# Kernel optimization log

Hardware: AMD Instinct MI355X
Metric: run time of the kernel (lower is better)

## Reference

```python
import math
import jax, jax.numpy as jnp
import numpy as np

D_MODEL = 1024
NUM_HEADS = 16
HEAD_DIM = D_MODEL // NUM_HEADS
BATCH = 4
SEQ = 2048


def setup_inputs() -> dict:
    key = jax.random.key(0)
    ks = jax.random.split(key, 9)
    scale = 1.0 / math.sqrt(D_MODEL)
    return {
        "x": jax.random.normal(ks[0], (BATCH, SEQ, D_MODEL), dtype=jnp.float32),
        "wq": jax.random.normal(ks[1], (D_MODEL, D_MODEL), dtype=jnp.float32) * scale,
        "bq": jnp.zeros((D_MODEL,), dtype=jnp.float32),
        "wk": jax.random.normal(ks[2], (D_MODEL, D_MODEL), dtype=jnp.float32) * scale,
        "bk": jnp.zeros((D_MODEL,), dtype=jnp.float32),
        "wv": jax.random.normal(ks[3], (D_MODEL, D_MODEL), dtype=jnp.float32) * scale,
        "bv": jnp.zeros((D_MODEL,), dtype=jnp.float32),
        "wo": jax.random.normal(ks[4], (D_MODEL, D_MODEL), dtype=jnp.float32) * scale,
        "bo": jnp.zeros((D_MODEL,), dtype=jnp.float32),
    }


def _split_heads(t):
    b, s, _ = t.shape
    return t.reshape(b, s, NUM_HEADS, HEAD_DIM).transpose(0, 2, 1, 3)  # [b,h,s,d]


def reference(x, wq, bq, wk, bk, wv, bv, wo, bo):
    # Linear layers: y = x @ W^T + b (torch nn.Linear convention)
    q = _split_heads(x @ wq.T + bq)
    k = _split_heads(x @ wk.T + bk)
    v = _split_heads(x @ wv.T + bv)
    scores = jnp.einsum("bhqd,bhkd->bhqk", q, k) / math.sqrt(HEAD_DIM)
    attn_weights = jax.nn.softmax(scores, axis=-1)  # dropout=0.0 (eval) -> identity
    context = jnp.einsum("bhqk,bhkd->bhqd", attn_weights, v)
    context = context.transpose(0, 2, 1, 3).reshape(x.shape[0], x.shape[1], D_MODEL)
    output = context @ wo.T + bo
    return output, attn_weights
```

## Files before the change

### kernel.cpp

```cpp
#include <hip/hip_runtime.h>
#include <cstdint>
#include <cstddef>


#define D_MODEL 1024
#define NHEADS  16
#define HDIM    64
#define BATCH   4
#define SEQ     2048
#define NTOK    (BATCH*SEQ)

typedef __bf16 bf16x8 __attribute__((ext_vector_type(8)));
typedef float  f32x4  __attribute__((ext_vector_type(4)));
typedef unsigned short u16x8 __attribute__((ext_vector_type(8)));

__device__ __forceinline__ uint16_t f2bf(float f) {
  union { float f; uint32_t u; } v; v.f = f;
  return (uint16_t)((v.u + 0x7FFFu + ((v.u >> 16) & 1u)) >> 16);
}
__device__ __forceinline__ float bf2f(uint16_t u) {
  union { uint32_t u; float f; } v; v.u = (uint32_t)u << 16; return v.f;
}
__device__ __forceinline__ bf16x8 ldbf8(const uint16_t* p) {
  return __builtin_bit_cast(bf16x8, *(const u16x8*)p);
}
__device__ __forceinline__ void nt_store4(float* p, float a, float b, float c, float d) {
  f32x4 v = { a, b, c, d };
  __builtin_nontemporal_store(v, (f32x4*)p);
}
#define MFMA16(a, b, c) __builtin_amdgcn_mfma_f32_16x16x32_bf16((a), (b), (c), 0, 0, 0)

__device__ __forceinline__ void gl_lds16(const uint16_t* g, uint16_t* l) {
  __builtin_amdgcn_global_load_lds(
      (const __attribute__((address_space(1))) uint32_t*)g,
      (__attribute__((address_space(3))) uint32_t*)l, 16, 0, 0);
}

__global__ __launch_bounds__(256) void cvt_kernel(const float* __restrict__ src,
                                                  uint16_t* __restrict__ dst, int n4) {
  int i = blockIdx.x * blockDim.x + threadIdx.x;
  if (i < n4) {
    float4 f = ((const float4*)src)[i];
    ushort4 o;
    o.x = f2bf(f.x); o.y = f2bf(f.y); o.z = f2bf(f.z); o.w = f2bf(f.w);
    ((ushort4*)dst)[i] = o;
  }
}
__global__ __launch_bounds__(256)
void cvt_w_kernel(const float* __restrict__ wq, const float* __restrict__ wk,
                  const float* __restrict__ wv, const float* __restrict__ wo,
                  uint16_t* __restrict__ dst) {
  int i = blockIdx.x * blockDim.x + threadIdx.x;
  int sel = i >> 18, off = i & 262143;
  const float* src = (sel == 0) ? wq : (sel == 1) ? wk : (sel == 2) ? wv : wo;
  float4 f = ((const float4*)src)[off];
  ushort4 o;
  o.x = f2bf(f.x); o.y = f2bf(f.y); o.z = f2bf(f.z); o.w = f2bf(f.w);
  ((ushort4*)dst)[i] = o;
}

__global__ __launch_bounds__(256)
void gemm_qkv(const uint16_t* __restrict__ A, const uint16_t* __restrict__ Wqkv,
              const float* __restrict__ bq, const float* __restrict__ bk,
              const float* __restrict__ bv,
              uint16_t* __restrict__ Qb, uint16_t* __restrict__ Kc,
              uint16_t* __restrict__ Vt) {
  __shared__ uint16_t As[128 * 64];
  __shared__ uint16_t Bs[128 * 64];
  const int flat = blockIdx.x;
  const int l = (flat & 7) * 192 + (flat >> 3);
  const int bx = l % 24, by = l / 24;
  const int tid  = threadIdx.x;
  const int lane = tid & 63;
  const int wave = tid >> 6;
  const int wr = wave >> 1, wc = wave & 1;
  const int m0 = by * 128, n0 = bx * 128;
  const int lrow = lane & 15;
  const int grp  = lane >> 4;
  const int l8   = lane >> 3;
  const int c8   = lane & 7;

  f32x4 acc[4][4] = {};

  for (int k0 = 0; k0 < 1024; k0 += 64) {
#pragma unroll
    for (int it = 0; it < 4; ++it) {
      const int chunk = wave * 4 + it;
      const int row = chunk * 8 + l8;
      gl_lds16(&A   [(size_t)(m0 + row) * 1024 + k0 + c8 * 8], &As[chunk * 512]);
      gl_lds16(&Wqkv[(size_t)(n0 + row) * 1024 + k0 + c8 * 8], &Bs[chunk * 512]);
    }
    __syncthreads();
#pragma unroll
    for (int ks = 0; ks < 2; ++ks) {
      bf16x8 af[4], bfr[4];
#pragma unroll
      for (int i = 0; i < 4; ++i) {
        af [i] = ldbf8(&As[(wr * 64 + i * 16 + lrow) * 64 + ks * 32 + grp * 8]);
        bfr[i] = ldbf8(&Bs[(wc * 64 + i * 16 + lrow) * 64 + ks * 32 + grp * 8]);
      }
#pragma unroll
      for (int i = 0; i < 4; ++i)
#pragma unroll
        for (int j = 0; j < 4; ++j)
          acc[i][j] = MFMA16(af[i], bfr[j], acc[i][j]);
    }
    __syncthreads();
  }

  const int seg = n0 >> 10;
  const float* bp = (seg == 0) ? bq : (seg == 1) ? bk : bv;
  uint16_t* dst01 = (seg == 0) ? Qb : Kc;
  const int r0 = grp * 4;
#pragma unroll
  for (int i = 0; i < 4; ++i) {
#pragma unroll
    for (int j = 0; j < 4; ++j) {
      int gmb = m0 + wr * 64 + i * 16 + r0;
      int gn  = n0 + wc * 64 + j * 16 + lrow;
      int nloc = gn & 1023;
      float bv_ = bp[nloc];
#pragma unroll
      for (int r = 0; r < 4; ++r) {
        float v = acc[i][j][r] + bv_;
        int gm = gmb + r;
        if (seg < 2) {
          dst01[(size_t)gm * 1024 + nloc] = f2bf(v);
        } else {
          int b = gm >> 11, s = gm & (SEQ - 1);
          int h = nloc >> 6, d = nloc & (HDIM - 1);
          Vt[(((size_t)(b * NHEADS + h) * HDIM + d) << 11) + s] = f2bf(v);
        }
      }
    }
  }
}

__global__ __launch_bounds__(256)
void gemm_out(const uint16_t* __restrict__ A, const uint16_t* __restrict__ Bt,
              const float* __restrict__ bias, float* __restrict__ out) {
  __shared__ uint16_t As[128 * 64];
  __shared__ uint16_t Bs[128 * 64];
  const int flat = blockIdx.x;
  const int l = (flat & 7) * 64 + (flat >> 3);
  const int bx = l & 7, by = l >> 3;
  const int tid  = threadIdx.x;
  const int lane = tid & 63;
  const int wave = tid >> 6;
  const int wr = wave >> 1, wc = wave & 1;
  const int m0 = by * 128, n0 = bx * 128;
  const int lrow = lane & 15;
  const int grp  = lane >> 4;
  const int l8   = lane >> 3;
  const int c8   = lane & 7;

  f32x4 acc[4][4] = {};

  for (int k0 = 0; k0 < 1024; k0 += 64) {
#pragma unroll
    for (int it = 0; it < 4; ++it) {
      const int chunk = wave * 4 + it;
      const int row = chunk * 8 + l8;
      gl_lds16(&A [(size_t)(m0 + row) * 1024 + k0 + c8 * 8], &As[chunk * 512]);
      gl_lds16(&Bt[(size_t)(n0 + row) * 1024 + k0 + c8 * 8], &Bs[chunk * 512]);
    }
    __syncthreads();
#pragma unroll
    for (int ks = 0; ks < 2; ++ks) {
      bf16x8 af[4], bfr[4];
#pragma unroll
      for (int i = 0; i < 4; ++i) {
        af [i] = ldbf8(&As[(wr * 64 + i * 16 + lrow) * 64 + ks * 32 + grp * 8]);
        bfr[i] = ldbf8(&Bs[(wc * 64 + i * 16 + lrow) * 64 + ks * 32 + grp * 8]);
      }
#pragma unroll
      for (int i = 0; i < 4; ++i)
#pragma unroll
        for (int j = 0; j < 4; ++j)
          acc[i][j] = MFMA16(af[i], bfr[j], acc[i][j]);
    }
    __syncthreads();
  }

  const int r0 = grp * 4;
#pragma unroll
  for (int i = 0; i < 4; ++i) {
#pragma unroll
    for (int j = 0; j < 4; ++j) {
      int gmb = m0 + wr * 64 + i * 16 + r0;
      int gn  = n0 + wc * 64 + j * 16 + lrow;
      float bv = bias[gn];
#pragma unroll
      for (int r = 0; r < 4; ++r)
        __builtin_nontemporal_store(acc[i][j][r] + bv,
                                    &out[(size_t)(gmb + r) * 1024 + gn]);
    }
  }
}

__device__ __forceinline__ bf16x8 rd_tile(const uint16_t* t, int r, int s) {
  return ldbf8(&t[r * 64 + ((s ^ (r & 7)) * 8)]);
}

#define QBLK 128
__global__ __launch_bounds__(512)
void attn_kernel(const uint16_t* __restrict__ Q, const uint16_t* __restrict__ Kb,
                 const uint16_t* __restrict__ Vt, float* __restrict__ attnw,
                 uint16_t* __restrict__ ctx) {
  __shared__ uint16_t Ks[2][64 * 64];
  __shared__ uint16_t Vs[2][64 * 64];
  __shared__ uint16_t Pl[8][16 * 72];
  const int tid  = threadIdx.x;
  const int lane = tid & 63;
  const int wave = tid >> 6;
  const int flat = blockIdx.x;
  const int lb = (flat & 7) * 128 + (flat >> 3);
  const int qt = lb & 15, h = (lb >> 4) & 15, b = lb >> 8;
  const int q0 = qt * QBLK + wave * 16;
  const int lrow = lane & 15;
  const int grp  = lane >> 4;
  const float c = 0.125f * 1.44269504088896f;

  const uint16_t* Kh = Kb + (size_t)(b * SEQ) * D_MODEL + h * HDIM;
  const uint16_t* Vh = Vt + ((size_t)(b * NHEADS + h) * HDIM) * SEQ;

  const size_t qbase = ((size_t)(b * SEQ) + q0 + lrow) * D_MODEL + h * HDIM;
  const bf16x8 qf0 = ldbf8(&Q[qbase + grp * 8]);
  const bf16x8 qf1 = ldbf8(&Q[qbase + 32 + grp * 8]);

  const int srow = wave * 8 + (lane >> 3);
  const int scb  = (lane & 7) ^ (srow & 7);

  float m = -INFINITY, l = 0.f;
  gl_lds16(&Kh[(size_t)srow * D_MODEL + scb * 8], &Ks[0][wave * 512]);
#pragma unroll 1
  for (int kc = 0; kc < SEQ / 64; ++kc) {
    const int cur = kc & 1;
    __syncthreads();
    if (kc + 1 < SEQ / 64)
      gl_lds16(&Kh[(size_t)((kc + 1) * 64 + srow) * D_MODEL + scb * 8],
               &Ks[cur ^ 1][wave * 512]);
    const uint16_t* kt_ = Ks[cur];
    f32x4 s[4];
#pragma unroll
    for (int kt = 0; kt < 4; ++kt) {
      f32x4 a = {};
      a = MFMA16(rd_tile(kt_, kt * 16 + lrow, grp),     qf0, a);
      a = MFMA16(rd_tile(kt_, kt * 16 + lrow, 4 + grp), qf1, a);
      s[kt] = a;
    }
    float v[16];
#pragma unroll
    for (int kt = 0; kt < 4; ++kt)
#pragma unroll
      for (int r = 0; r < 4; ++r) v[kt * 4 + r] = s[kt][r] * c;
    float mx = v[0];
#pragma unroll
    for (int i = 1; i < 16; ++i) mx = fmaxf(mx, v[i]);
    float mn = fmaxf(m, mx);
    float sum = 0.f;
#pragma unroll
    for (int i = 0; i < 16; ++i) sum += __builtin_amdgcn_exp2f(v[i] - mn);
    l = l * __builtin_amdgcn_exp2f(m - mn) + sum;
    m = mn;
  }
#pragma unroll
  for (int d = 16; d <= 32; d <<= 1) {
    float mp = __shfl_xor(m, d), lp = __shfl_xor(l, d);
    float mn = fmaxf(m, mp);
    l = l * __builtin_amdgcn_exp2f(m - mn) + lp * __builtin_amdgcn_exp2f(mp - mn);
    m = mn;
  }
  const float rinv = 1.0f / l;

  f32x4 cacc[4] = {};
  uint16_t* pw = &Pl[wave][0];
  float* awc = attnw + (((size_t)(b * NHEADS + h)) * SEQ + q0) * SEQ;
  gl_lds16(&Kh[(size_t)srow * D_MODEL + scb * 8], &Ks[0][wave * 512]);
  gl_lds16(&Vh[(size_t)srow * SEQ + scb * 8],     &Vs[0][wave * 512]);
#pragma unroll 1
  for (int kc = 0; kc < SEQ / 64; ++kc) {
    const int cur = kc & 1;
    __syncthreads();
    if (kc + 1 < SEQ / 64) {
      gl_lds16(&Kh[(size_t)((kc + 1) * 64 + srow) * D_MODEL + scb * 8],
               &Ks[cur ^ 1][wave * 512]);
      gl_lds16(&Vh[(size_t)srow * SEQ + (kc + 1) * 64 + scb * 8],
               &Vs[cur ^ 1][wave * 512]);
    }
    const uint16_t* kt_ = Ks[cur];
    f32x4 s[4];
#pragma unroll
    for (int kt = 0; kt < 4; ++kt) {
      f32x4 a = {};
      a = MFMA16(rd_tile(kt_, kt * 16 + lrow, grp),     qf0, a);
      a = MFMA16(rd_tile(kt_, kt * 16 + lrow, 4 + grp), qf1, a);
      s[kt] = a;
    }
#pragma unroll
    for (int kt = 0; kt < 4; ++kt) {
      ushort4 w;
      w.x = f2bf(__builtin_amdgcn_exp2f(s[kt][0] * c - m) * rinv);
      w.y = f2bf(__builtin_amdgcn_exp2f(s[kt][1] * c - m) * rinv);
      w.z = f2bf(__builtin_amdgcn_exp2f(s[kt][2] * c - m) * rinv);
      w.w = f2bf(__builtin_amdgcn_exp2f(s[kt][3] * c - m) * rinv);
      *(ushort4*)&pw[lrow * 72 + kt * 16 + grp * 4] = w;
    }
    asm volatile("s_waitcnt lgkmcnt(0)" ::: "memory");
#pragma unroll
    for (int ii = 0; ii < 4; ++ii) {
      int q = ii * 4 + grp;
      ushort4 t4 = *(const ushort4*)&pw[q * 72 + lrow * 4];
      nt_store4(&awc[(size_t)q * SEQ + kc * 64 + lrow * 4],
                bf2f(t4.x), bf2f(t4.y), bf2f(t4.z), bf2f(t4.w));
    }
    const uint16_t* vt_ = Vs[cur];
#pragma unroll
    for (int ks = 0; ks < 2; ++ks) {
      const bf16x8 pf = ldbf8(&pw[lrow * 72 + ks * 32 + grp * 8]);
#pragma unroll
      for (int n = 0; n < 4; ++n) {
        const bf16x8 vf = rd_tile(vt_, n * 16 + lrow, ks * 4 + grp);
        cacc[n] = MFMA16(pf, vf, cacc[n]);
      }
    }
  }
#pragma unroll
  for (int n = 0; n < 4; ++n)
#pragma unroll
    for (int r = 0; r < 4; ++r) {
      int gq = q0 + grp * 4 + r;
      ctx[((size_t)(b * SEQ) + gq) * D_MODEL + h * HDIM + n * 16 + lrow] = f2bf(cacc[n][r]);
    }
}

extern "C" void kernel_launch(void* const* d_in, const int* in_sizes, int n_in,
                              void* d_out, int out_size, void* d_ws, size_t ws_size,
                              hipStream_t stream) {
  const float* x  = (const float*)d_in[0];
  const float* wq = (const float*)d_in[1];
  const float* bq = (const float*)d_in[2];
  const float* wk = (const float*)d_in[3];
  const float* bk = (const float*)d_in[4];
  const float* wv = (const float*)d_in[5];
  const float* bv = (const float*)d_in[6];
  const float* wo = (const float*)d_in[7];
  const float* bo = (const float*)d_in[8];

  char* ws = (char*)d_ws;
  uint16_t* xb   = (uint16_t*)ws;
  uint16_t* wqkv = (uint16_t*)(ws + (16u << 20));
  uint16_t* wob  = (uint16_t*)(ws + (22u << 20));
  uint16_t* Qb   = (uint16_t*)(ws + (24u << 20));
  uint16_t* Kc   = (uint16_t*)(ws + (40u << 20));
  uint16_t* Vtb  = (uint16_t*)(ws + (56u << 20));
  uint16_t* ctx  = xb;

  float* outp  = (float*)d_out;
  float* attnw = outp + (size_t)NTOK * D_MODEL;

  {
    int n4 = (NTOK * D_MODEL) / 4;
    cvt_kernel<<<(n4 + 255) / 256, 256, 0, stream>>>(x, xb, n4);
    cvt_w_kernel<<<(4 * 262144) / 256, 256, 0, stream>>>(wq, wk, wv, wo, wqkv);
  }

  gemm_qkv<<<1536, 256, 0, stream>>>(xb, wqkv, bq, bk, bv, Qb, Kc, Vtb);

  attn_kernel<<<1024, 512, 0, stream>>>(Qb, Kc, Vtb, attnw, ctx);

  gemm_out<<<512, 256, 0, stream>>>(ctx, wob, bo, outp);
}
```

Measured before the change: 388.1 us.

## Double query rows per wave in attention to reuse K/V tiles

Each wave now handles 32 query rows (two 16-row groups) instead of 16, so the block covers 256 queries and the grid halves to 512 blocks. Each K and V tile staged in shared memory is reused for twice as many MFMAs, cutting global K/V traffic and LDS loads per query. The cost is more registers per thread, a larger P buffer in LDS, and fewer blocks, which could reduce occupancy or leave CUs underused on the 256-CU part.

```diff
diff --git a/kernel.cpp b/kernel.cpp
--- a/kernel.cpp
+++ b/kernel.cpp
@@ -202,21 +202,21 @@
   return ldbf8(&t[r * 64 + ((s ^ (r & 7)) * 8)]);
 }
 
-#define QBLK 128
+#define QBLK 256
 __global__ __launch_bounds__(512)
 void attn_kernel(const uint16_t* __restrict__ Q, const uint16_t* __restrict__ Kb,
                  const uint16_t* __restrict__ Vt, float* __restrict__ attnw,
                  uint16_t* __restrict__ ctx) {
   __shared__ uint16_t Ks[2][64 * 64];
   __shared__ uint16_t Vs[2][64 * 64];
-  __shared__ uint16_t Pl[8][16 * 72];
+  __shared__ uint16_t Pl[8][32 * 72];
   const int tid  = threadIdx.x;
   const int lane = tid & 63;
   const int wave = tid >> 6;
   const int flat = blockIdx.x;
-  const int lb = (flat & 7) * 128 + (flat >> 3);
-  const int qt = lb & 15, h = (lb >> 4) & 15, b = lb >> 8;
-  const int q0 = qt * QBLK + wave * 16;
+  const int lb = (flat & 7) * 64 + (flat >> 3);
+  const int qt = lb & 7, h = (lb >> 3) & 15, b = lb >> 7;
+  const int q0 = qt * QBLK + wave * 32;
   const int lrow = lane & 15;
   const int grp  = lane >> 4;
   const float c = 0.125f * 1.44269504088896f;
@@ -224,14 +224,18 @@
   const uint16_t* Kh = Kb + (size_t)(b * SEQ) * D_MODEL + h * HDIM;
   const uint16_t* Vh = Vt + ((size_t)(b * NHEADS + h) * HDIM) * SEQ;
 
-  const size_t qbase = ((size_t)(b * SEQ) + q0 + lrow) * D_MODEL + h * HDIM;
-  const bf16x8 qf0 = ldbf8(&Q[qbase + grp * 8]);
-  const bf16x8 qf1 = ldbf8(&Q[qbase + 32 + grp * 8]);
+  bf16x8 qf[2][2];
+#pragma unroll
+  for (int g = 0; g < 2; ++g) {
+    const size_t qb = ((size_t)(b * SEQ) + q0 + g * 16 + lrow) * D_MODEL + h * HDIM;
+    qf[g][0] = ldbf8(&Q[qb + grp * 8]);
+    qf[g][1] = ldbf8(&Q[qb + 32 + grp * 8]);
+  }
 
   const int srow = wave * 8 + (lane >> 3);
   const int scb  = (lane & 7) ^ (srow & 7);
 
-  float m = -INFINITY, l = 0.f;
+  float m[2] = { -INFINITY, -INFINITY }, l[2] = { 0.f, 0.f };
   gl_lds16(&Kh[(size_t)srow * D_MODEL + scb * 8], &Ks[0][wave * 512]);
 #pragma unroll 1
   for (int kc = 0; kc < SEQ / 64; ++kc) {
@@ -241,39 +245,46 @@
       gl_lds16(&Kh[(size_t)((kc + 1) * 64 + srow) * D_MODEL + scb * 8],
                &Ks[cur ^ 1][wave * 512]);
     const uint16_t* kt_ = Ks[cur];
-    f32x4 s[4];
-#pragma unroll
-    for (int kt = 0; kt < 4; ++kt) {
-      f32x4 a = {};
-      a = MFMA16(rd_tile(kt_, kt * 16 + lrow, grp),     qf0, a);
-      a = MFMA16(rd_tile(kt_, kt * 16 + lrow, 4 + grp), qf1, a);
-      s[kt] = a;
-    }
-    float v[16];
-#pragma unroll
-    for (int kt = 0; kt < 4; ++kt)
-#pragma unroll
-      for (int r = 0; r < 4; ++r) v[kt * 4 + r] = s[kt][r] * c;
-    float mx = v[0];
-#pragma unroll
-    for (int i = 1; i < 16; ++i) mx = fmaxf(mx, v[i]);
-    float mn = fmaxf(m, mx);
-    float sum = 0.f;
-#pragma unroll
-    for (int i = 0; i < 16; ++i) sum += __builtin_amdgcn_exp2f(v[i] - mn);
-    l = l * __builtin_amdgcn_exp2f(m - mn) + sum;
-    m = mn;
-  }
-#pragma unroll
-  for (int d = 16; d <= 32; d <<= 1) {
-    float mp = __shfl_xor(m, d), lp = __shfl_xor(l, d);
-    float mn = fmaxf(m, mp);
-    l = l * __builtin_amdgcn_exp2f(m - mn) + lp * __builtin_amdgcn_exp2f(mp - mn);
-    m = mn;
-  }
-  const float rinv = 1.0f / l;
-
-  f32x4 cacc[4] = {};
+#pragma unroll
+    for (int g = 0; g < 2; ++g) {
+      f32x4 s[4];
+#pragma unroll
+      for (int kt = 0; kt < 4; ++kt) {
+        f32x4 a = {};
+        a = MFMA16(rd_tile(kt_, kt * 16 + lrow, grp),     qf[g][0], a);
+        a = MFMA16(rd_tile(kt_, kt * 16 + lrow, 4 + grp), qf[g][1], a);
+        s[kt] = a;
+      }
+      float v[16];
+#pragma unroll
+      for (int kt = 0; kt < 4; ++kt)
+#pragma unroll
+        for (int r = 0; r < 4; ++r) v[kt * 4 + r] = s[kt][r] * c;
+      float mx = v[0];
+#pragma unroll
+      for (int i = 1; i < 16; ++i) mx = fmaxf(mx, v[i]);
+      float mn = fmaxf(m[g], mx);
+      float sum = 0.f;
+#pragma unroll
+      for (int i = 0; i < 16; ++i) sum += __builtin_amdgcn_exp2f(v[i] - mn);
+      l[g] = l[g] * __builtin_amdgcn_exp2f(m[g] - mn) + sum;
+      m[g] = mn;
+    }
+  }
+  float rinv[2];
+#pragma unroll
+  for (int g = 0; g < 2; ++g) {
+#pragma unroll
+    for (int d = 16; d <= 32; d <<= 1) {
+      float mp = __shfl_xor(m[g], d), lp = __shfl_xor(l[g], d);
+      float mn = fmaxf(m[g], mp);
+      l[g] = l[g] * __builtin_amdgcn_exp2f(m[g] - mn) + lp * __builtin_amdgcn_exp2f(mp - mn);
+      m[g] = mn;
+    }
+    rinv[g] = 1.0f / l[g];
+  }
+
+  f32x4 cacc[2][4] = {};
   uint16_t* pw = &Pl[wave][0];
   float* awc = attnw + (((size_t)(b * NHEADS + h)) * SEQ + q0) * SEQ;
   gl_lds16(&Kh[(size_t)srow * D_MODEL + scb * 8], &Ks[0][wave * 512]);
@@ -289,49 +300,58 @@
                &Vs[cur ^ 1][wave * 512]);
     }
     const uint16_t* kt_ = Ks[cur];
-    f32x4 s[4];
-#pragma unroll
-    for (int kt = 0; kt < 4; ++kt) {
-      f32x4 a = {};
-      a = MFMA16(rd_tile(kt_, kt * 16 + lrow, grp),     qf0, a);
-      a = MFMA16(rd_tile(kt_, kt * 16 + lrow, 4 + grp), qf1, a);
-      s[kt] = a;
-    }
-#pragma unroll
-    for (int kt = 0; kt < 4; ++kt) {
-      ushort4 w;
-      w.x = f2bf(__builtin_amdgcn_exp2f(s[kt][0] * c - m) * rinv);
-      w.y = f2bf(__builtin_amdgcn_exp2f(s[kt][1] * c - m) * rinv);
-      w.z = f2bf(__builtin_amdgcn_exp2f(s[kt][2] * c - m) * rinv);
-      w.w = f2bf(__builtin_amdgcn_exp2f(s[kt][3] * c - m) * rinv);
-      *(ushort4*)&pw[lrow * 72 + kt * 16 + grp * 4] = w;
+#pragma unroll
+    for (int g = 0; g < 2; ++g) {
+      f32x4 s[4];
+#pragma unroll
+      for (int kt = 0; kt < 4; ++kt) {
+        f32x4 a = {};
+        a = MFMA16(rd_tile(kt_, kt * 16 + lrow, grp),     qf[g][0], a);
+        a = MFMA16(rd_tile(kt_, kt * 16 + lrow, 4 + grp), qf[g][1], a);
+        s[kt] = a;
+      }
+#pragma unroll
+      for (int kt = 0; kt < 4; ++kt) {
+        ushort4 w;
+        w.x = f2bf(__builtin_amdgcn_exp2f(s[kt][0] * c - m[g]) * rinv[g]);
+        w.y = f2bf(__builtin_amdgcn_exp2f(s[kt][1] * c - m[g]) * rinv[g]);
+        w.z = f2bf(__builtin_amdgcn_exp2f(s[kt][2] * c - m[g]) * rinv[g]);
+        w.w = f2bf(__builtin_amdgcn_exp2f(s[kt][3] * c - m[g]) * rinv[g]);
+        *(ushort4*)&pw[(g * 16 + lrow) * 72 + kt * 16 + grp * 4] = w;
+      }
     }
     asm volatile("s_waitcnt lgkmcnt(0)" ::: "memory");
 #pragma unroll
-    for (int ii = 0; ii < 4; ++ii) {
-      int q = ii * 4 + grp;
-      ushort4 t4 = *(const ushort4*)&pw[q * 72 + lrow * 4];
-      nt_store4(&awc[(size_t)q * SEQ + kc * 64 + lrow * 4],
-                bf2f(t4.x), bf2f(t4.y), bf2f(t4.z), bf2f(t4.w));
-    }
+    for (int g = 0; g < 2; ++g)
+#pragma unroll
+      for (int ii = 0; ii < 4; ++ii) {
+        int q = g * 16 + ii * 4 + grp;
+        ushort4 t4 = *(const ushort4*)&pw[q * 72 + lrow * 4];
+        nt_store4(&awc[(size_t)q * SEQ + kc * 64 + lrow * 4],
+                  bf2f(t4.x), bf2f(t4.y), bf2f(t4.z), bf2f(t4.w));
+      }
     const uint16_t* vt_ = Vs[cur];
 #pragma unroll
     for (int ks = 0; ks < 2; ++ks) {
-      const bf16x8 pf = ldbf8(&pw[lrow * 72 + ks * 32 + grp * 8]);
+      bf16x8 pf0 = ldbf8(&pw[(lrow)      * 72 + ks * 32 + grp * 8]);
+      bf16x8 pf1 = ldbf8(&pw[(16 + lrow) * 72 + ks * 32 + grp * 8]);
 #pragma unroll
       for (int n = 0; n < 4; ++n) {
         const bf16x8 vf = rd_tile(vt_, n * 16 + lrow, ks * 4 + grp);
-        cacc[n] = MFMA16(pf, vf, cacc[n]);
-      }
-    }
-  }
-#pragma unroll
-  for (int n = 0; n < 4; ++n)
-#pragma unroll
-    for (int r = 0; r < 4; ++r) {
-      int gq = q0 + grp * 4 + r;
-      ctx[((size_t)(b * SEQ) + gq) * D_MODEL + h * HDIM + n * 16 + lrow] = f2bf(cacc[n][r]);
-    }
+        cacc[0][n] = MFMA16(pf0, vf, cacc[0][n]);
+        cacc[1][n] = MFMA16(pf1, vf, cacc[1][n]);
+      }
+    }
+  }
+#pragma unroll
+  for (int g = 0; g < 2; ++g)
+#pragma unroll
+    for (int n = 0; n < 4; ++n)
+#pragma unroll
+      for (int r = 0; r < 4; ++r) {
+        int gq = q0 + g * 16 + grp * 4 + r;
+        ctx[((size_t)(b * SEQ) + gq) * D_MODEL + h * HDIM + n * 16 + lrow] = f2bf(cacc[g][n][r]);
+      }
 }
 
 extern "C" void kernel_launch(void* const* d_in, const int* in_sizes, int n_in,
@@ -367,7 +387,7 @@
 
   gemm_qkv<<<1536, 256, 0, stream>>>(xb, wqkv, bq, bk, bv, Qb, Kc, Vtb);
 
-  attn_kernel<<<1024, 512, 0, stream>>>(Qb, Kc, Vtb, attnw, ctx);
+  attn_kernel<<<512, 512, 0, stream>>>(Qb, Kc, Vtb, attnw, ctx);
 
   gemm_out<<<512, 256, 0, stream>>>(ctx, wob, bo, outp);
 }
```

Result: no change. 388.9 us (+0.2%).
